# Performance work log

Hardware: AMD Instinct MI355X
Metric: run time of the kernel (lower is better)

Reference implementation:

```python
import jax, jax.numpy as jnp
import numpy as np

GROUPS = 32
EPS = 1e-5


def group_norm(x, scale, bias):
    # x: [B,H,W,C]; stats over (H, W, channels-within-group)
    B, H, W, C = x.shape
    xg = x.reshape(B, H, W, GROUPS, C // GROUPS)
    mean = xg.mean(axis=(1, 2, 4), keepdims=True)
    var = xg.var(axis=(1, 2, 4), keepdims=True)
    xn = ((xg - mean) * jax.lax.rsqrt(var + EPS)).reshape(B, H, W, C)
    return xn * scale + bias


def conv1x1(x, w, b):
    # 1x1 conv == per-pixel matmul; w: [C_in, C_out]
    return jnp.einsum('bhwc,cd->bhwd', x, w) + b


def setup_inputs() -> dict:
    key = jax.random.key(0)
    ks = jax.random.split(key, 10)
    B, H, W, C = 8, 64, 64, 512
    bound = np.sqrt(3.0 / C)  # variance_scaling(1.0, fan_in, uniform)
    x = jax.random.normal(ks[0], (B, H, W, C), dtype=jnp.float32)
    wq = jax.random.uniform(ks[1], (C, C), jnp.float32, -bound, bound)
    wk = jax.random.uniform(ks[2], (C, C), jnp.float32, -bound, bound)
    wv = jax.random.uniform(ks[3], (C, C), jnp.float32, -bound, bound)
    wp = jnp.zeros((C, C), jnp.float32)  # proj_out init scale=0.0
    bq = jnp.zeros((C,), jnp.float32)
    bk = jnp.zeros((C,), jnp.float32)
    bv = jnp.zeros((C,), jnp.float32)
    bp = jnp.zeros((C,), jnp.float32)
    gn_scale = jnp.ones((C,), jnp.float32)
    gn_bias = jnp.zeros((C,), jnp.float32)
    return {"x": x, "wq": wq, "bq": bq, "wk": wk, "bk": bk, "wv": wv,
            "bv": bv, "wp": wp, "bp": bp, "gn_scale": gn_scale, "gn_bias": gn_bias}


def reference(x, wq, bq, wk, bk, wv, bv, wp, bp, gn_scale, gn_bias):
    B, H, W, C = x.shape
    h = group_norm(x, gn_scale, gn_bias)
    q = conv1x1(h, wq, bq).reshape(B, H * W, C)
    k = conv1x1(h, wk, bk).reshape(B, H * W, C)
    v = conv1x1(h, wv, bv).reshape(B, H * W, C)
    # contraction over spatial dim j=H*W -> channel attention [B, C, C]
    attn = jnp.einsum('bji,bjk->bik', q, k)
    attn = jax.nn.softmax(attn, axis=-1)
    h = jnp.einsum('bij,bkj->bik', v, attn)  # [B, HW, C]
    h = h.reshape(B, H, W, C)
    h = conv1x1(h, wp, bp)
    return x + h
```

## Files before the change

### kernel.cpp

```cpp
#include <hip/hip_runtime.h>
#include <hip/hip_bf16.h>


using bf16   = __bf16;
using bf16x8 = __attribute__((ext_vector_type(8))) __bf16;
using bf16x4 = __attribute__((ext_vector_type(4))) __bf16;
using f32x4  = __attribute__((ext_vector_type(4))) float;

#define DI __device__ __forceinline__

DI void gemm128_core(const bf16* __restrict__ A, long lda,
                     const bf16* __restrict__ B, long ldb,
                     int ksteps, bf16* As, bf16* Bs, f32x4 acc[4][4]) {
  const int tid  = threadIdx.x;
  const int lane = tid & 63;
  const int w    = tid >> 6;
  const int lr   = lane & 15;
  const int lk   = (lane >> 4) * 8;
  const int wr   = (w >> 1) * 64;
  const int wc   = (w & 1) * 64;
  const int sw   = (lr & 7) << 3;

  for (int kt = 0; kt < ksteps; ++kt) {
    bf16x8 av[4], bv[4];
#pragma unroll
    for (int c = 0; c < 4; ++c) {
      const int idx = c * 256 + tid;
      const int row = idx >> 3, col = (idx & 7) * 8;
      av[c] = *(const bf16x8*)(A + (long)row * lda + (long)kt * 64 + col);
      bv[c] = *(const bf16x8*)(B + (long)row * ldb + (long)kt * 64 + col);
    }
#pragma unroll
    for (int c = 0; c < 4; ++c) {
      const int idx = c * 256 + tid;
      const int row = idx >> 3;
      const int scol = ((idx & 7) * 8) ^ ((row & 7) << 3);
      *(bf16x8*)(As + row * 64 + scol) = av[c];
      *(bf16x8*)(Bs + row * 64 + scol) = bv[c];
    }
    __syncthreads();
#pragma unroll
    for (int kk = 0; kk < 2; ++kk) {
      bf16x8 af[4], bfr[4];
#pragma unroll
      for (int i = 0; i < 4; ++i)
        af[i] = *(const bf16x8*)(As + (wr + i * 16 + lr) * 64 + ((kk * 32 + lk) ^ sw));
#pragma unroll
      for (int i = 0; i < 4; ++i)
        bfr[i] = *(const bf16x8*)(Bs + (wc + i * 16 + lr) * 64 + ((kk * 32 + lk) ^ sw));
#pragma unroll
      for (int i = 0; i < 4; ++i)
#pragma unroll
        for (int j = 0; j < 4; ++j)
          acc[i][j] = __builtin_amdgcn_mfma_f32_16x16x32_bf16(af[i], bfr[j], acc[i][j], 0, 0, 0);
    }
    __syncthreads();
  }
}

DI void gemm64_core(const bf16* __restrict__ A, long lda,
                    const bf16* __restrict__ B, long ldb,
                    int ksteps, bf16* As, bf16* Bs, f32x4 acc[2][2]) {
  const int tid  = threadIdx.x;
  const int lane = tid & 63;
  const int w    = tid >> 6;
  const int lr   = lane & 15;
  const int lk   = (lane >> 4) * 8;
  const int wr   = (w >> 1) * 32;
  const int wc   = (w & 1) * 32;
  const int sw   = (lr & 7) << 3;

  for (int kt = 0; kt < ksteps; ++kt) {
    bf16x8 av[2], bv[2];
#pragma unroll
    for (int c = 0; c < 2; ++c) {
      const int idx = c * 256 + tid;
      const int row = idx >> 3, col = (idx & 7) * 8;
      av[c] = *(const bf16x8*)(A + (long)row * lda + (long)kt * 64 + col);
      bv[c] = *(const bf16x8*)(B + (long)row * ldb + (long)kt * 64 + col);
    }
#pragma unroll
    for (int c = 0; c < 2; ++c) {
      const int idx = c * 256 + tid;
      const int row = idx >> 3;
      const int scol = ((idx & 7) * 8) ^ ((row & 7) << 3);
      *(bf16x8*)(As + row * 64 + scol) = av[c];
      *(bf16x8*)(Bs + row * 64 + scol) = bv[c];
    }
    __syncthreads();
#pragma unroll
    for (int kk = 0; kk < 2; ++kk) {
      bf16x8 af[2], bfr[2];
#pragma unroll
      for (int i = 0; i < 2; ++i)
        af[i] = *(const bf16x8*)(As + (wr + i * 16 + lr) * 64 + ((kk * 32 + lk) ^ sw));
#pragma unroll
      for (int i = 0; i < 2; ++i)
        bfr[i] = *(const bf16x8*)(Bs + (wc + i * 16 + lr) * 64 + ((kk * 32 + lk) ^ sw));
#pragma unroll
      for (int i = 0; i < 2; ++i)
#pragma unroll
        for (int j = 0; j < 2; ++j)
          acc[i][j] = __builtin_amdgcn_mfma_f32_16x16x32_bf16(af[i], bfr[j], acc[i][j], 0, 0, 0);
    }
    __syncthreads();
  }
}

__global__ __launch_bounds__(256) void k_gnstats(const float* __restrict__ x,
                                                 float2* __restrict__ stats) {
  const int bg = blockIdx.x, b = bg >> 5, g = bg & 31;
  const float* base = x + (size_t)b * 4096 * 512 + g * 16;
  const int tid = threadIdx.x;
  float s = 0.f, ss = 0.f;
  for (int it = 0; it < 64; ++it) {
    const int idx = it * 256 + tid;
    const int p = idx >> 2, c4 = (idx & 3) * 4;
    float4 v = *(const float4*)(base + (size_t)p * 512 + c4);
    s  += v.x + v.y + v.z + v.w;
    ss += v.x * v.x + v.y * v.y + v.z * v.z + v.w * v.w;
  }
  __shared__ float rs[256], rss[256];
  rs[tid] = s; rss[tid] = ss; __syncthreads();
  for (int off = 128; off; off >>= 1) {
    if (tid < off) { rs[tid] += rs[tid + off]; rss[tid] += rss[tid + off]; }
    __syncthreads();
  }
  if (tid == 0) {
    float mean = rs[0] * (1.f / 65536.f);
    float var  = rss[0] * (1.f / 65536.f) - mean * mean;
    stats[bg] = float2{mean, rsqrtf(var + 1e-5f)};
  }
}

__global__ __launch_bounds__(256) void k_gnapply_t(const float* __restrict__ x,
                                                   const float2* __restrict__ stats,
                                                   const float* __restrict__ gns,
                                                   const float* __restrict__ gnb,
                                                   bf16* __restrict__ Hn,
                                                   bf16* __restrict__ HnT,
                                                   float* __restrict__ s) {
  __shared__ bf16 tile[64 * 516];
  __shared__ float cs[512];
  const int tid = threadIdx.x;
  const int blk = blockIdx.x;
  const int b = blk >> 6, p0 = (blk & 63) * 64;
  cs[tid] = 0.f; cs[tid + 256] = 0.f;
  __syncthreads();

  const int c4 = (tid & 127) * 4;
  const int hi = tid >> 7;
  const float2 st = stats[b * 32 + (c4 >> 4)];
  const float4 sc = *(const float4*)(gns + c4);
  const float4 bi = *(const float4*)(gnb + c4);
  float a0 = 0.f, a1 = 0.f, a2 = 0.f, a3 = 0.f;
  for (int i = 0; i < 32; ++i) {
    const int px = i * 2 + hi;
    const float4 xv = *(const float4*)(x + ((size_t)(b * 4096 + p0 + px)) * 512 + c4);
    const float h0 = (xv.x - st.x) * st.y * sc.x + bi.x;
    const float h1 = (xv.y - st.x) * st.y * sc.y + bi.y;
    const float h2 = (xv.z - st.x) * st.y * sc.z + bi.z;
    const float h3 = (xv.w - st.x) * st.y * sc.w + bi.w;
    a0 += h0; a1 += h1; a2 += h2; a3 += h3;
    bf16x4 hv;
    hv[0] = (bf16)h0; hv[1] = (bf16)h1; hv[2] = (bf16)h2; hv[3] = (bf16)h3;
    *(bf16x4*)(Hn + ((size_t)(b * 4096 + p0 + px)) * 512 + c4) = hv;
    *(bf16x4*)(tile + px * 516 + c4) = hv;
  }
  atomicAdd(&cs[c4 + 0], a0); atomicAdd(&cs[c4 + 1], a1);
  atomicAdd(&cs[c4 + 2], a2); atomicAdd(&cs[c4 + 3], a3);
  __syncthreads();
  atomicAdd(s + b * 512 + tid, cs[tid]);
  atomicAdd(s + b * 512 + 256 + tid, cs[tid + 256]);

  for (int cg = 0; cg < 16; ++cg) {
    const int c  = cg * 32 + (tid >> 3);
    const int so = (tid & 7) * 8;
    bf16x8 pk;
#pragma unroll
    for (int k = 0; k < 8; ++k) pk[k] = tile[(so + k) * 516 + c];
    *(bf16x8*)(HnT + ((size_t)(b * 512 + c)) * 4096 + p0 + so) = pk;
  }
}

__global__ void k_wt(const float* __restrict__ wq, const float* __restrict__ wk,
                     const float* __restrict__ wv, const float* __restrict__ wp,
                     bf16* __restrict__ WT, bf16* __restrict__ wvb,
                     float* __restrict__ s) {
  __shared__ float t[32][33];
  const int z = blockIdx.z;
  const float* src = (z == 0) ? wq : (z == 1) ? wk : (z == 2) ? wv : wp;
  const int n0 = blockIdx.x * 32, k0 = blockIdx.y * 32;
  const int tx = threadIdx.x, ty = threadIdx.y;
  if (z == 0 && blockIdx.y == 0) s[blockIdx.x * 256 + ty * 32 + tx] = 0.f;
#pragma unroll
  for (int j = 0; j < 4; ++j) {
    const float v = src[(size_t)(k0 + ty + j * 8) * 512 + n0 + tx];
    t[ty + j * 8][tx] = v;
    if (z == 2) wvb[(size_t)(k0 + ty + j * 8) * 512 + n0 + tx] = (bf16)v;
  }
  __syncthreads();
#pragma unroll
  for (int j = 0; j < 4; ++j)
    WT[(size_t)(z * 512 + n0 + ty + j * 8) * 512 + k0 + tx] = (bf16)t[tx][ty + j * 8];
}

__global__ __launch_bounds__(256) void k_gram(const bf16* __restrict__ HnT,
                                              float* __restrict__ part) {
  __shared__ bf16 As[128 * 64], Bs[128 * 64];
  const int Lb = blockIdx.x;
  const int b  = Lb & 7;
  const int idx = Lb >> 3;
  const int sp = idx & 3;
  const int t  = idx >> 2;
  const int m0 = (int)((0x3221110000ull >> (4 * t)) & 15) * 128;
  const int n0 = (int)((0x3323213210ull >> (4 * t)) & 15) * 128;
  f32x4 acc[4][4];
#pragma unroll
  for (int i = 0; i < 4; ++i)
#pragma unroll
    for (int j = 0; j < 4; ++j) acc[i][j] = (f32x4){0.f, 0.f, 0.f, 0.f};
  const bf16* A = HnT + ((size_t)b * 512 + m0) * 4096 + sp * 1024;
  const bf16* B = HnT + ((size_t)b * 512 + n0) * 4096 + sp * 1024;
  gemm128_core(A, 4096, B, 4096, 16, As, Bs, acc);

  const int lane = threadIdx.x & 63, w = threadIdx.x >> 6;
  const int wr = (w >> 1) * 64, wc = (w & 1) * 64;
  const int rr = (lane >> 4) * 4, cc = lane & 15;
  float* dst = part + (size_t)(sp * 8 + b) * 262144;
#pragma unroll
  for (int i = 0; i < 4; ++i) {
#pragma unroll
    for (int j = 0; j < 4; ++j) {
      const int gm = m0 + wr + i * 16 + rr;
      const int gn = n0 + wc + j * 16 + cc;
      float* p = dst + (size_t)gm * 512 + gn;
      p[0]    = acc[i][j][0];
      p[512]  = acc[i][j][1];
      p[1024] = acc[i][j][2];
      p[1536] = acc[i][j][3];
      if (m0 != n0)
        *(f32x4*)(dst + (size_t)gn * 512 + gm) = acc[i][j];
    }
  }
}

__global__ __launch_bounds__(256) void k_gsum(const float* __restrict__ part,
                                              bf16* __restrict__ G) {
  const size_t S8 = (size_t)8 * 262144;
  const size_t i4 = ((size_t)blockIdx.x * 256 + threadIdx.x) * 4;
  const float4 a = *(const float4*)(part + i4);
  const float4 c = *(const float4*)(part + i4 + S8);
  const float4 d = *(const float4*)(part + i4 + 2 * S8);
  const float4 e = *(const float4*)(part + i4 + 3 * S8);
  bf16x4 o;
  o[0] = (bf16)(a.x + c.x + d.x + e.x); o[1] = (bf16)(a.y + c.y + d.y + e.y);
  o[2] = (bf16)(a.z + c.z + d.z + e.z); o[3] = (bf16)(a.w + c.w + d.w + e.w);
  *(bf16x4*)(G + i4) = o;
}

__global__ __launch_bounds__(512) void k_vecs(const bf16* __restrict__ WT,
                                              const float* __restrict__ s,
                                              const float* __restrict__ bv,
                                              const bf16* __restrict__ T,
                                              float* __restrict__ uq,
                                              float* __restrict__ vkv,
                                              float* __restrict__ dv,
                                              int mode) {
  const int i = threadIdx.x;
  if (mode == 0) {
    const int z = blockIdx.x;
    const int which = z >> 3, b = z & 7;
    const bf16* row = WT + ((size_t)(which * 512 + i)) * 512;
    const float* sv = s + b * 512;
    float acc = 0.f;
    for (int c = 0; c < 512; ++c) acc += (float)row[c] * sv[c];
    (which == 0 ? uq : vkv)[b * 512 + i] = acc;
  } else {
    const int b = blockIdx.x;
    const bf16* row = T + (size_t)b * 262144 + (size_t)i * 512;
    float acc = 0.f;
    for (int c = 0; c < 512; ++c) acc += (float)row[c] * bv[c];
    dv[b * 512 + i] = acc;
  }
}

__global__ __launch_bounds__(256) void k_sg64_bf(const bf16* __restrict__ Ab, long a_bs,
                                                 const bf16* __restrict__ Bb, long b_bs,
                                                 bf16* __restrict__ Cb) {
  __shared__ bf16 As[64 * 64], Bs[64 * 64];
  const int b = blockIdx.z;
  const int m0 = blockIdx.y * 64, n0 = blockIdx.x * 64;
  f32x4 acc[2][2];
#pragma unroll
  for (int i = 0; i < 2; ++i)
#pragma unroll
    for (int j = 0; j < 2; ++j) acc[i][j] = (f32x4){0.f, 0.f, 0.f, 0.f};
  gemm64_core(Ab + (size_t)b * a_bs + (size_t)m0 * 512, 512,
              Bb + (size_t)b * b_bs + (size_t)n0 * 512, 512, 8, As, Bs, acc);

  const int lane = threadIdx.x & 63, w = threadIdx.x >> 6;
  const int wr = (w >> 1) * 32, wc = (w & 1) * 32;
  const int rr = (lane >> 4) * 4, cc = lane & 15;
  bf16* dst = Cb + (size_t)b * 262144;
#pragma unroll
  for (int i = 0; i < 2; ++i) {
#pragma unroll
    for (int j = 0; j < 2; ++j) {
      const int gm = m0 + wr + i * 16 + rr;
      const int gn = n0 + wc + j * 16 + cc;
      bf16* p = dst + (size_t)gm * 512 + gn;
      p[0]    = (bf16)acc[i][j][0];
      p[512]  = (bf16)acc[i][j][1];
      p[1024] = (bf16)acc[i][j][2];
      p[1536] = (bf16)acc[i][j][3];
    }
  }
}

__global__ __launch_bounds__(256) void k_sg64_f32(const bf16* __restrict__ Ab, long a_bs,
                                                  const bf16* __restrict__ Bb, long b_bs,
                                                  float* __restrict__ Cb) {
  __shared__ bf16 As[64 * 64], Bs[64 * 64];
  const int b = blockIdx.z;
  const int m0 = blockIdx.y * 64, n0 = blockIdx.x * 64;
  f32x4 acc[2][2];
#pragma unroll
  for (int i = 0; i < 2; ++i)
#pragma unroll
    for (int j = 0; j < 2; ++j) acc[i][j] = (f32x4){0.f, 0.f, 0.f, 0.f};
  gemm64_core(Ab + (size_t)b * a_bs + (size_t)m0 * 512, 512,
              Bb + (size_t)b * b_bs + (size_t)n0 * 512, 512, 8, As, Bs, acc);

  const int lane = threadIdx.x & 63, w = threadIdx.x >> 6;
  const int wr = (w >> 1) * 32, wc = (w & 1) * 32;
  const int rr = (lane >> 4) * 4, cc = lane & 15;
  float* dst = Cb + (size_t)b * 262144;
#pragma unroll
  for (int i = 0; i < 2; ++i) {
#pragma unroll
    for (int j = 0; j < 2; ++j) {
      const int gm = m0 + wr + i * 16 + rr;
      const int gn = n0 + wc + j * 16 + cc;
      float* p = dst + (size_t)gm * 512 + gn;
      p[0]    = acc[i][j][0];
      p[512]  = acc[i][j][1];
      p[1024] = acc[i][j][2];
      p[1536] = acc[i][j][3];
    }
  }
}

__global__ __launch_bounds__(128) void k_softmax(const float* __restrict__ L,
                                                 const float* __restrict__ uq,
                                                 const float* __restrict__ vkv,
                                                 const float* __restrict__ bq,
                                                 const float* __restrict__ bk,
                                                 bf16* __restrict__ attn) {
  const int row = blockIdx.x, tid = threadIdx.x;
  const int b = row >> 9, i = row & 511;
  const float r  = uq[b * 512 + i];
  const float q0 = bq[i];
  const float4 l  = *(const float4*)(L + (size_t)row * 512 + tid * 4);
  const float4 bk4 = *(const float4*)(bk + tid * 4);
  const float4 vk4 = *(const float4*)(vkv + b * 512 + tid * 4);
  const float v0 = l.x + r * bk4.x + q0 * (vk4.x + 4096.f * bk4.x);
  const float v1 = l.y + r * bk4.y + q0 * (vk4.y + 4096.f * bk4.y);
  const float v2 = l.z + r * bk4.z + q0 * (vk4.z + 4096.f * bk4.z);
  const float v3 = l.w + r * bk4.w + q0 * (vk4.w + 4096.f * bk4.w);
  __shared__ float red[128];
  red[tid] = fmaxf(fmaxf(v0, v1), fmaxf(v2, v3));
  __syncthreads();
  for (int off = 64; off; off >>= 1) {
    if (tid < off) red[tid] = fmaxf(red[tid], red[tid + off]);
    __syncthreads();
  }
  const float M = red[0];
  __syncthreads();
  const float e0 = __expf(v0 - M), e1 = __expf(v1 - M);
  const float e2 = __expf(v2 - M), e3 = __expf(v3 - M);
  red[tid] = e0 + e1 + e2 + e3;
  __syncthreads();
  for (int off = 64; off; off >>= 1) {
    if (tid < off) red[tid] += red[tid + off];
    __syncthreads();
  }
  const float inv = 1.f / red[0];
  bf16x4 o;
  o[0] = (bf16)(e0 * inv); o[1] = (bf16)(e1 * inv);
  o[2] = (bf16)(e2 * inv); o[3] = (bf16)(e3 * inv);
  *(bf16x4*)(attn + (size_t)row * 512 + tid * 4) = o;
}

__global__ void k_att_t(const bf16* __restrict__ attn, bf16* __restrict__ attnT) {
  __shared__ bf16 t[32][33];
  const int b = blockIdx.z;
  const int n0 = blockIdx.x * 32, k0 = blockIdx.y * 32;
  const int tx = threadIdx.x, ty = threadIdx.y;
#pragma unroll
  for (int j = 0; j < 4; ++j)
    t[ty + j * 8][tx] = attn[(size_t)b * 262144 + (size_t)(k0 + ty + j * 8) * 512 + n0 + tx];
  __syncthreads();
#pragma unroll
  for (int j = 0; j < 4; ++j)
    attnT[(size_t)b * 262144 + (size_t)(n0 + ty + j * 8) * 512 + k0 + tx] = t[tx][ty + j * 8];
}

__global__ __launch_bounds__(256) void k_final(const bf16* __restrict__ Hn,
                                               const bf16* __restrict__ CT,
                                               const float* __restrict__ dv,
                                               const float* __restrict__ bp,
                                               const float* __restrict__ x,
                                               float* __restrict__ out) {
  __shared__ bf16 As[128 * 64], Bs[128 * 64];
  const int Lb = blockIdx.x;
  const int b  = Lb & 7;
  const int idx = Lb >> 3;
  const int m0 = (idx >> 2) * 128;
  const int n0 = (idx & 3) * 128;
  f32x4 acc[4][4];
#pragma unroll
  for (int i = 0; i < 4; ++i)
#pragma unroll
    for (int j = 0; j < 4; ++j) acc[i][j] = (f32x4){0.f, 0.f, 0.f, 0.f};
  gemm128_core(Hn + ((size_t)b * 4096 + m0) * 512, 512,
               CT + (size_t)b * 262144 + (size_t)n0 * 512, 512, 8, As, Bs, acc);

  const int lane = threadIdx.x & 63, w = threadIdx.x >> 6;
  const int wr = (w >> 1) * 64, wc = (w & 1) * 64;
  const int rr = (lane >> 4) * 4, cc = lane & 15;
#pragma unroll
  for (int i = 0; i < 4; ++i) {
#pragma unroll
    for (int j = 0; j < 4; ++j) {
      const int gm = m0 + wr + i * 16 + rr;
      const int gn = n0 + wc + j * 16 + cc;
      const float add = dv[b * 512 + gn] + bp[gn];
#pragma unroll
      for (int jj = 0; jj < 4; ++jj) {
        const size_t off = ((size_t)(b * 4096 + gm + jj)) * 512 + gn;
        out[off] = acc[i][j][jj] + add + x[off];
      }
    }
  }
}

extern "C" void kernel_launch(void* const* d_in, const int* in_sizes, int n_in,
                              void* d_out, int out_size, void* d_ws, size_t ws_size,
                              hipStream_t stream) {
  const float* x   = (const float*)d_in[0];
  const float* wq  = (const float*)d_in[1];
  const float* bq  = (const float*)d_in[2];
  const float* wk  = (const float*)d_in[3];
  const float* bk  = (const float*)d_in[4];
  const float* wv  = (const float*)d_in[5];
  const float* bv  = (const float*)d_in[6];
  const float* wp  = (const float*)d_in[7];
  const float* bp  = (const float*)d_in[8];
  const float* gns = (const float*)d_in[9];
  const float* gnb = (const float*)d_in[10];
  float* out = (float*)d_out;

  const size_t MB = 1ull << 20;
  const size_t KB = 1024;
  char* wsb = (char*)d_ws;
  bf16*   WT    = (bf16*)(wsb);
  bf16*   wvb   = (bf16*)(wsb + 2 * MB);
  float2* stats = (float2*)(wsb + 2 * MB + 512 * KB);
  float*  s     = (float*)(wsb + 2 * MB + 576 * KB);
  float*  uq    = (float*)(wsb + 2 * MB + 640 * KB);
  float*  vkv   = (float*)(wsb + 2 * MB + 704 * KB);
  float*  dv    = (float*)(wsb + 2 * MB + 768 * KB);
  bf16*   Hn    = (bf16*)(wsb + 3 * MB);
  bf16*   HnT   = (bf16*)(wsb + 35 * MB);
  float*  part  = (float*)(wsb + 67 * MB);
  bf16*   attn  = (bf16*)(wsb + 67 * MB);
  bf16*   attnT = (bf16*)(wsb + 71 * MB);
  bf16*   T     = (bf16*)(wsb + 75 * MB);
  bf16*   CT    = (bf16*)(wsb + 79 * MB);
  bf16*   G     = (bf16*)(wsb + 99 * MB);
  bf16*   M1    = (bf16*)(wsb + 103 * MB);
  float*  L     = (float*)(wsb + 107 * MB);

  const long S2 = 512 * 512;

  k_wt        <<<dim3(16, 16, 4), dim3(32, 8), 0, stream>>>(wq, wk, wv, wp, WT, wvb, s);
  k_gnstats   <<<dim3(256),       dim3(256),   0, stream>>>(x, stats);
  k_gnapply_t <<<dim3(512),       dim3(256),   0, stream>>>(x, stats, gns, gnb, Hn, HnT, s);
  k_gram      <<<dim3(320),       dim3(256),   0, stream>>>(HnT, part);
  k_gsum      <<<dim3(2048),      dim3(256),   0, stream>>>(part, G);
  k_vecs      <<<dim3(16),        dim3(512),   0, stream>>>(WT, s, bv, T, uq, vkv, dv, 0);
  k_sg64_bf   <<<dim3(8, 8, 8),   dim3(256),   0, stream>>>(WT, 0, G, S2, M1);
  k_sg64_f32  <<<dim3(8, 8, 8),   dim3(256),   0, stream>>>(M1, S2, WT + (size_t)512 * 512, 0, L);
  k_softmax   <<<dim3(4096),      dim3(128),   0, stream>>>(L, uq, vkv, bq, bk, attn);
  k_att_t     <<<dim3(16, 16, 8), dim3(32, 8), 0, stream>>>(attn, attnT);
  k_sg64_bf   <<<dim3(8, 8, 8),   dim3(256),   0, stream>>>(WT + (size_t)3 * 512 * 512, 0, attnT, S2, T);
  k_vecs      <<<dim3(8),         dim3(512),   0, stream>>>(WT, s, bv, T, uq, vkv, dv, 1);
  k_sg64_bf   <<<dim3(8, 8, 8),   dim3(256),   0, stream>>>(T, S2, wvb, 0, CT);
  k_final     <<<dim3(1024),      dim3(256),   0, stream>>>(Hn, CT, dv, bp, x, out);
}
```

Baseline: 195.7 us.

## Fuse prep, gsum/vecs, softmax+transpose; recompute normalized input in final GEMM

Merges the weight transpose and group-norm stats into one launch, folds the row-sum vector products into the G reduction launch, and fuses softmax with the attention transpose while also computing the attn·bv bias term. The final kernel no longer reads a stored bf16 normalized tensor. It recomputes the group-norm from x on the fly and computes the projected bias per block, so the Hn write is dropped. Fewer launches and less global traffic, at the cost of redundant per-block bias dot products and extra fp32 x reads in the final GEMM.

```diff
diff --git a/kernel.cpp b/kernel.cpp
--- a/kernel.cpp
+++ b/kernel.cpp
@@ -107,29 +107,59 @@
   }
 }
 
-__global__ __launch_bounds__(256) void k_gnstats(const float* __restrict__ x,
-                                                 float2* __restrict__ stats) {
-  const int bg = blockIdx.x, b = bg >> 5, g = bg & 31;
-  const float* base = x + (size_t)b * 4096 * 512 + g * 16;
+__global__ __launch_bounds__(256) void k_prep(const float* __restrict__ x,
+                                              const float* __restrict__ wq,
+                                              const float* __restrict__ wk,
+                                              const float* __restrict__ wv,
+                                              const float* __restrict__ wp,
+                                              bf16* __restrict__ WT,
+                                              bf16* __restrict__ wvb,
+                                              float* __restrict__ s,
+                                              float2* __restrict__ stats) {
+  __shared__ float shm[1056];
   const int tid = threadIdx.x;
-  float s = 0.f, ss = 0.f;
-  for (int it = 0; it < 64; ++it) {
-    const int idx = it * 256 + tid;
-    const int p = idx >> 2, c4 = (idx & 3) * 4;
-    float4 v = *(const float4*)(base + (size_t)p * 512 + c4);
-    s  += v.x + v.y + v.z + v.w;
-    ss += v.x * v.x + v.y * v.y + v.z * v.z + v.w * v.w;
-  }
-  __shared__ float rs[256], rss[256];
-  rs[tid] = s; rss[tid] = ss; __syncthreads();
-  for (int off = 128; off; off >>= 1) {
-    if (tid < off) { rs[tid] += rs[tid + off]; rss[tid] += rss[tid + off]; }
-    __syncthreads();
-  }
-  if (tid == 0) {
-    float mean = rs[0] * (1.f / 65536.f);
-    float var  = rss[0] * (1.f / 65536.f) - mean * mean;
-    stats[bg] = float2{mean, rsqrtf(var + 1e-5f)};
+  const int bx = blockIdx.x;
+  if (bx < 256) {
+    const int b = bx >> 5, g = bx & 31;
+    const float* base = x + (size_t)b * 4096 * 512 + g * 16;
+    float sm = 0.f, ss = 0.f;
+    for (int it = 0; it < 64; ++it) {
+      const int idx = it * 256 + tid;
+      const int p = idx >> 2, c4 = (idx & 3) * 4;
+      float4 v = *(const float4*)(base + (size_t)p * 512 + c4);
+      sm += v.x + v.y + v.z + v.w;
+      ss += v.x * v.x + v.y * v.y + v.z * v.z + v.w * v.w;
+    }
+    float* rs = shm; float* rss = shm + 256;
+    rs[tid] = sm; rss[tid] = ss; __syncthreads();
+    for (int off = 128; off; off >>= 1) {
+      if (tid < off) { rs[tid] += rs[tid + off]; rss[tid] += rss[tid + off]; }
+      __syncthreads();
+    }
+    if (tid == 0) {
+      float mean = rs[0] * (1.f / 65536.f);
+      float var  = rss[0] * (1.f / 65536.f) - mean * mean;
+      stats[bx] = float2{mean, rsqrtf(var + 1e-5f)};
+    }
+  } else {
+    const int r = bx - 256;
+    const int z = r >> 8;
+    const int r2 = r & 255;
+    const int bxx = r2 & 15, byy = r2 >> 4;
+    const int tx = tid & 31, ty = tid >> 5;
+    const float* src = (z == 0) ? wq : (z == 1) ? wk : (z == 2) ? wv : wp;
+    const int n0 = bxx * 32, k0 = byy * 32;
+    if (z == 0 && byy == 0) s[bxx * 256 + tid] = 0.f;
+#pragma unroll
+    for (int j = 0; j < 4; ++j) {
+      const float v = src[(size_t)(k0 + ty + j * 8) * 512 + n0 + tx];
+      shm[(ty + j * 8) * 33 + tx] = v;
+      if (z == 2) wvb[(size_t)(k0 + ty + j * 8) * 512 + n0 + tx] = (bf16)v;
+    }
+    __syncthreads();
+#pragma unroll
+    for (int j = 0; j < 4; ++j)
+      WT[(size_t)(z * 512 + n0 + ty + j * 8) * 512 + k0 + tx] = (bf16)shm[tx * 33 + ty + j * 8];
   }
 }
 
@@ -137,7 +167,6 @@
                                                    const float2* __restrict__ stats,
                                                    const float* __restrict__ gns,
                                                    const float* __restrict__ gnb,
-                                                   bf16* __restrict__ Hn,
                                                    bf16* __restrict__ HnT,
                                                    float* __restrict__ s) {
   __shared__ bf16 tile[64 * 516];
@@ -164,7 +193,6 @@
     a0 += h0; a1 += h1; a2 += h2; a3 += h3;
     bf16x4 hv;
     hv[0] = (bf16)h0; hv[1] = (bf16)h1; hv[2] = (bf16)h2; hv[3] = (bf16)h3;
-    *(bf16x4*)(Hn + ((size_t)(b * 4096 + p0 + px)) * 512 + c4) = hv;
     *(bf16x4*)(tile + px * 516 + c4) = hv;
   }
   atomicAdd(&cs[c4 + 0], a0); atomicAdd(&cs[c4 + 1], a1);
@@ -181,28 +209,6 @@
     for (int k = 0; k < 8; ++k) pk[k] = tile[(so + k) * 516 + c];
     *(bf16x8*)(HnT + ((size_t)(b * 512 + c)) * 4096 + p0 + so) = pk;
   }
-}
-
-__global__ void k_wt(const float* __restrict__ wq, const float* __restrict__ wk,
-                     const float* __restrict__ wv, const float* __restrict__ wp,
-                     bf16* __restrict__ WT, bf16* __restrict__ wvb,
-                     float* __restrict__ s) {
-  __shared__ float t[32][33];
-  const int z = blockIdx.z;
-  const float* src = (z == 0) ? wq : (z == 1) ? wk : (z == 2) ? wv : wp;
-  const int n0 = blockIdx.x * 32, k0 = blockIdx.y * 32;
-  const int tx = threadIdx.x, ty = threadIdx.y;
-  if (z == 0 && blockIdx.y == 0) s[blockIdx.x * 256 + ty * 32 + tx] = 0.f;
-#pragma unroll
-  for (int j = 0; j < 4; ++j) {
-    const float v = src[(size_t)(k0 + ty + j * 8) * 512 + n0 + tx];
-    t[ty + j * 8][tx] = v;
-    if (z == 2) wvb[(size_t)(k0 + ty + j * 8) * 512 + n0 + tx] = (bf16)v;
-  }
-  __syncthreads();
-#pragma unroll
-  for (int j = 0; j < 4; ++j)
-    WT[(size_t)(z * 512 + n0 + ty + j * 8) * 512 + k0 + tx] = (bf16)t[tx][ty + j * 8];
 }
 
 __global__ __launch_bounds__(256) void k_gram(const bf16* __restrict__ HnT,
@@ -245,43 +251,41 @@
   }
 }
 
-__global__ __launch_bounds__(256) void k_gsum(const float* __restrict__ part,
-                                              bf16* __restrict__ G) {
-  const size_t S8 = (size_t)8 * 262144;
-  const size_t i4 = ((size_t)blockIdx.x * 256 + threadIdx.x) * 4;
-  const float4 a = *(const float4*)(part + i4);
-  const float4 c = *(const float4*)(part + i4 + S8);
-  const float4 d = *(const float4*)(part + i4 + 2 * S8);
-  const float4 e = *(const float4*)(part + i4 + 3 * S8);
-  bf16x4 o;
-  o[0] = (bf16)(a.x + c.x + d.x + e.x); o[1] = (bf16)(a.y + c.y + d.y + e.y);
-  o[2] = (bf16)(a.z + c.z + d.z + e.z); o[3] = (bf16)(a.w + c.w + d.w + e.w);
-  *(bf16x4*)(G + i4) = o;
-}
-
-__global__ __launch_bounds__(512) void k_vecs(const bf16* __restrict__ WT,
-                                              const float* __restrict__ s,
-                                              const float* __restrict__ bv,
-                                              const bf16* __restrict__ T,
-                                              float* __restrict__ uq,
-                                              float* __restrict__ vkv,
-                                              float* __restrict__ dv,
-                                              int mode) {
-  const int i = threadIdx.x;
-  if (mode == 0) {
-    const int z = blockIdx.x;
+__global__ __launch_bounds__(256) void k_gsumv(const float* __restrict__ part,
+                                               bf16* __restrict__ G,
+                                               const bf16* __restrict__ WT,
+                                               const float* __restrict__ s,
+                                               float* __restrict__ uq,
+                                               float* __restrict__ vkv) {
+  const int bx = blockIdx.x, tid = threadIdx.x;
+  if (bx < 2048) {
+    const size_t S8 = (size_t)8 * 262144;
+    const size_t i4 = ((size_t)bx * 256 + tid) * 4;
+    const float4 a = *(const float4*)(part + i4);
+    const float4 c = *(const float4*)(part + i4 + S8);
+    const float4 d = *(const float4*)(part + i4 + 2 * S8);
+    const float4 e = *(const float4*)(part + i4 + 3 * S8);
+    bf16x4 o;
+    o[0] = (bf16)(a.x + c.x + d.x + e.x); o[1] = (bf16)(a.y + c.y + d.y + e.y);
+    o[2] = (bf16)(a.z + c.z + d.z + e.z); o[3] = (bf16)(a.w + c.w + d.w + e.w);
+    *(bf16x4*)(G + i4) = o;
+  } else {
+    const int z = bx - 2048;
     const int which = z >> 3, b = z & 7;
-    const bf16* row = WT + ((size_t)(which * 512 + i)) * 512;
     const float* sv = s + b * 512;
-    float acc = 0.f;
-    for (int c = 0; c < 512; ++c) acc += (float)row[c] * sv[c];
-    (which == 0 ? uq : vkv)[b * 512 + i] = acc;
-  } else {
-    const int b = blockIdx.x;
-    const bf16* row = T + (size_t)b * 262144 + (size_t)i * 512;
-    float acc = 0.f;
-    for (int c = 0; c < 512; ++c) acc += (float)row[c] * bv[c];
-    dv[b * 512 + i] = acc;
+    for (int o = tid; o < 512; o += 256) {
+      const bf16* row = WT + ((size_t)(which * 512 + o)) * 512;
+      float acc = 0.f;
+      for (int c = 0; c < 512; c += 8) {
+        bf16x8 v = *(const bf16x8*)(row + c);
+        const float4 s0 = *(const float4*)(sv + c);
+        const float4 s1 = *(const float4*)(sv + c + 4);
+        acc += (float)v[0] * s0.x + (float)v[1] * s0.y + (float)v[2] * s0.z +
+               (float)v[3] * s0.w + (float)v[4] * s1.x + (float)v[5] * s1.y +
+               (float)v[6] * s1.z + (float)v[7] * s1.w;
+      }
+      (which == 0 ? uq : vkv)[b * 512 + o] = acc;
+    }
   }
 }
 
@@ -351,91 +355,180 @@
   }
 }
 
-__global__ __launch_bounds__(128) void k_softmax(const float* __restrict__ L,
-                                                 const float* __restrict__ uq,
-                                                 const float* __restrict__ vkv,
-                                                 const float* __restrict__ bq,
-                                                 const float* __restrict__ bk,
-                                                 bf16* __restrict__ attn) {
-  const int row = blockIdx.x, tid = threadIdx.x;
-  const int b = row >> 9, i = row & 511;
+__global__ __launch_bounds__(256) void k_smax(const float* __restrict__ L,
+                                              const float* __restrict__ uq,
+                                              const float* __restrict__ vkv,
+                                              const float* __restrict__ bq,
+                                              const float* __restrict__ bk,
+                                              const float* __restrict__ bv,
+                                              bf16* __restrict__ attnT,
+                                              float* __restrict__ attnbv) {
+  __shared__ bf16 p[4][512];
+  const int tid = threadIdx.x;
+  const int w = tid >> 6, l = tid & 63;
+  const int blk = blockIdx.x;
+  const int gr = blk * 4 + w;
+  const int b = gr >> 9, i = gr & 511;
+  const int c = l * 8;
+
   const float r  = uq[b * 512 + i];
   const float q0 = bq[i];
-  const float4 l  = *(const float4*)(L + (size_t)row * 512 + tid * 4);
-  const float4 bk4 = *(const float4*)(bk + tid * 4);
-  const float4 vk4 = *(const float4*)(vkv + b * 512 + tid * 4);
-  const float v0 = l.x + r * bk4.x + q0 * (vk4.x + 4096.f * bk4.x);
-  const float v1 = l.y + r * bk4.y + q0 * (vk4.y + 4096.f * bk4.y);
-  const float v2 = l.z + r * bk4.z + q0 * (vk4.z + 4096.f * bk4.z);
-  const float v3 = l.w + r * bk4.w + q0 * (vk4.w + 4096.f * bk4.w);
-  __shared__ float red[128];
-  red[tid] = fmaxf(fmaxf(v0, v1), fmaxf(v2, v3));
+  const float* lp = L + (size_t)gr * 512 + c;
+  const float4 l0 = *(const float4*)lp;
+  const float4 l1 = *(const float4*)(lp + 4);
+  const float4 k0 = *(const float4*)(bk + c);
+  const float4 k1 = *(const float4*)(bk + c + 4);
+  const float4 g0 = *(const float4*)(vkv + b * 512 + c);
+  const float4 g1 = *(const float4*)(vkv + b * 512 + c + 4);
+  float v[8];
+  v[0] = l0.x + r * k0.x + q0 * (g0.x + 4096.f * k0.x);
+  v[1] = l0.y + r * k0.y + q0 * (g0.y + 4096.f * k0.y);
+  v[2] = l0.z + r * k0.z + q0 * (g0.z + 4096.f * k0.z);
+  v[3] = l0.w + r * k0.w + q0 * (g0.w + 4096.f * k0.w);
+  v[4] = l1.x + r * k1.x + q0 * (g1.x + 4096.f * k1.x);
+  v[5] = l1.y + r * k1.y + q0 * (g1.y + 4096.f * k1.y);
+  v[6] = l1.z + r * k1.z + q0 * (g1.z + 4096.f * k1.z);
+  v[7] = l1.w + r * k1.w + q0 * (g1.w + 4096.f * k1.w);
+
+  float mx = v[0];
+#pragma unroll
+  for (int j = 1; j < 8; ++j) mx = fmaxf(mx, v[j]);
+  for (int off = 32; off; off >>= 1) mx = fmaxf(mx, __shfl_xor(mx, off));
+  float e[8], sm = 0.f;
+#pragma unroll
+  for (int j = 0; j < 8; ++j) { e[j] = __expf(v[j] - mx); sm += e[j]; }
+  for (int off = 32; off; off >>= 1) sm += __shfl_xor(sm, off);
+  const float inv = 1.f / sm;
+
+  const float4 b0 = *(const float4*)(bv + c);
+  const float4 b1 = *(const float4*)(bv + c + 4);
+  float ab = e[0] * b0.x + e[1] * b0.y + e[2] * b0.z + e[3] * b0.w +
+             e[4] * b1.x + e[5] * b1.y + e[6] * b1.z + e[7] * b1.w;
+  ab *= inv;
+  for (int off = 32; off; off >>= 1) ab += __shfl_xor(ab, off);
+  if (l == 0) attnbv[gr] = ab;
+
+  bf16x8 o;
+#pragma unroll
+  for (int j = 0; j < 8; ++j) o[j] = (bf16)(e[j] * inv);
+  *(bf16x8*)(&p[w][c]) = o;
   __syncthreads();
-  for (int off = 64; off; off >>= 1) {
-    if (tid < off) red[tid] = fmaxf(red[tid], red[tid + off]);
-    __syncthreads();
-  }
-  const float M = red[0];
-  __syncthreads();
-  const float e0 = __expf(v0 - M), e1 = __expf(v1 - M);
-  const float e2 = __expf(v2 - M), e3 = __expf(v3 - M);
-  red[tid] = e0 + e1 + e2 + e3;
-  __syncthreads();
-  for (int off = 64; off; off >>= 1) {
-    if (tid < off) red[tid] += red[tid + off];
-    __syncthreads();
-  }
-  const float inv = 1.f / red[0];
-  bf16x4 o;
-  o[0] = (bf16)(e0 * inv); o[1] = (bf16)(e1 * inv);
-  o[2] = (bf16)(e2 * inv); o[3] = (bf16)(e3 * inv);
-  *(bf16x4*)(attn + (size_t)row * 512 + tid * 4) = o;
-}
-
-__global__ void k_att_t(const bf16* __restrict__ attn, bf16* __restrict__ attnT) {
-  __shared__ bf16 t[32][33];
-  const int b = blockIdx.z;
-  const int n0 = blockIdx.x * 32, k0 = blockIdx.y * 32;
-  const int tx = threadIdx.x, ty = threadIdx.y;
-#pragma unroll
-  for (int j = 0; j < 4; ++j)
-    t[ty + j * 8][tx] = attn[(size_t)b * 262144 + (size_t)(k0 + ty + j * 8) * 512 + n0 + tx];
-  __syncthreads();
-#pragma unroll
-  for (int j = 0; j < 4; ++j)
-    attnT[(size_t)b * 262144 + (size_t)(n0 + ty + j * 8) * 512 + k0 + tx] = t[tx][ty + j * 8];
-}
-
-__global__ __launch_bounds__(256) void k_final(const bf16* __restrict__ Hn,
+
+  const int i0 = (blk * 4) & 511;
+  for (int n = tid; n < 512; n += 256) {
+    bf16x4 t;
+    t[0] = p[0][n]; t[1] = p[1][n]; t[2] = p[2][n]; t[3] = p[3][n];
+    *(bf16x4*)(attnT + (size_t)b * 262144 + (size_t)n * 512 + i0) = t;
+  }
+}
+
+__global__ __launch_bounds__(256) void k_final(const float* __restrict__ x,
                                                const bf16* __restrict__ CT,
-                                               const float* __restrict__ dv,
+                                               const float* __restrict__ attnbv,
+                                               const bf16* __restrict__ WTp,
+                                               const float* __restrict__ gns,
+                                               const float* __restrict__ gnb,
+                                               const float2* __restrict__ stats,
                                                const float* __restrict__ bp,
-                                               const float* __restrict__ x,
                                                float* __restrict__ out) {
   __shared__ bf16 As[128 * 64], Bs[128 * 64];
+  __shared__ float gsc[512], gbs[512], abvs[512], dvs[128];
   const int Lb = blockIdx.x;
   const int b  = Lb & 7;
   const int idx = Lb >> 3;
   const int m0 = (idx >> 2) * 128;
   const int n0 = (idx & 3) * 128;
+  const int tid = threadIdx.x;
+
+  for (int cch = tid; cch < 512; cch += 256) {
+    const float2 st = stats[b * 32 + (cch >> 4)];
+    const float a = st.y * gns[cch];
+    gsc[cch] = a;
+    gbs[cch] = gnb[cch] - st.x * a;
+    abvs[cch] = attnbv[b * 512 + cch];
+  }
+  __syncthreads();
+  if (tid < 128) {
+    const bf16* wrow = WTp + (size_t)(n0 + tid) * 512;
+    float acc = 0.f;
+    for (int k = 0; k < 512; k += 8) {
+      bf16x8 v = *(const bf16x8*)(wrow + k);
+#pragma unroll
+      for (int j = 0; j < 8; ++j) acc += (float)v[j] * abvs[k + j];
+    }
+    dvs[tid] = acc;
+  }
+
+  const int lane = tid & 63, w = tid >> 6;
+  const int lr = lane & 15, lk = (lane >> 4) * 8;
+  const int wr2 = (w >> 1) * 64, wc = (w & 1) * 64;
+  const int sw = (lr & 7) << 3;
   f32x4 acc[4][4];
 #pragma unroll
   for (int i = 0; i < 4; ++i)
 #pragma unroll
     for (int j = 0; j < 4; ++j) acc[i][j] = (f32x4){0.f, 0.f, 0.f, 0.f};
-  gemm128_core(Hn + ((size_t)b * 4096 + m0) * 512, 512,
-               CT + (size_t)b * 262144 + (size_t)n0 * 512, 512, 8, As, Bs, acc);
-
-  const int lane = threadIdx.x & 63, w = threadIdx.x >> 6;
-  const int wr = (w >> 1) * 64, wc = (w & 1) * 64;
+
+  const bf16* Bg = CT + (size_t)b * 262144 + (size_t)n0 * 512;
+  for (int kt = 0; kt < 8; ++kt) {
+    bf16x8 av[4], bv[4];
+#pragma unroll
+    for (int c = 0; c < 4; ++c) {
+      const int idx2 = c * 256 + tid;
+      const int row = idx2 >> 3;
+      const int ch  = kt * 64 + (idx2 & 7) * 8;
+      const float* xp = x + ((size_t)(b * 4096 + m0 + row)) * 512 + ch;
+      const float4 x0 = *(const float4*)xp;
+      const float4 x1 = *(const float4*)(xp + 4);
+      const float4 s0 = *(const float4*)(gsc + ch);
+      const float4 s1 = *(const float4*)(gsc + ch + 4);
+      const float4 c0 = *(const float4*)(gbs + ch);
+      const float4 c1 = *(const float4*)(gbs + ch + 4);
+      av[c][0] = (bf16)(x0.x * s0.x + c0.x);
+      av[c][1] = (bf16)(x0.y * s0.y + c0.y);
+      av[c][2] = (bf16)(x0.z * s0.z + c0.z);
+      av[c][3] = (bf16)(x0.w * s0.w + c0.w);
+      av[c][4] = (bf16)(x1.x * s1.x + c1.x);
+      av[c][5] = (bf16)(x1.y * s1.y + c1.y);
+      av[c][6] = (bf16)(x1.z * s1.z + c1.z);
+      av[c][7] = (bf16)(x1.w * s1.w + c1.w);
+      bv[c] = *(const bf16x8*)(Bg + (size_t)row * 512 + ch);
+    }
+#pragma unroll
+    for (int c = 0; c < 4; ++c) {
+      const int idx2 = c * 256 + tid;
+      const int row = idx2 >> 3;
+      const int scol = ((idx2 & 7) * 8) ^ ((row & 7) << 3);
+      *(bf16x8*)(As + row * 64 + scol) = av[c];
+      *(bf16x8*)(Bs + row * 64 + scol) = bv[c];
+    }
+    __syncthreads();
+#pragma unroll
+    for (int kk = 0; kk < 2; ++kk) {
+      bf16x8 af[4], bfr[4];
+#pragma unroll
+      for (int i = 0; i < 4; ++i)
+        af[i] = *(const bf16x8*)(As + (wr2 + i * 16 + lr) * 64 + ((kk * 32 + lk) ^ sw));
+#pragma unroll
+      for (int i = 0; i < 4; ++i)
+        bfr[i] = *(const bf16x8*)(Bs + (wc + i * 16 + lr) * 64 + ((kk * 32 + lk) ^ sw));
+#pragma unroll
+      for (int i = 0; i < 4; ++i)
+#pragma unroll
+        for (int j = 0; j < 4; ++j)
+          acc[i][j] = __builtin_amdgcn_mfma_f32_16x16x32_bf16(af[i], bfr[j], acc[i][j], 0, 0, 0);
+    }
+    __syncthreads();
+  }
+
   const int rr = (lane >> 4) * 4, cc = lane & 15;
 #pragma unroll
   for (int i = 0; i < 4; ++i) {
 #pragma unroll
     for (int j = 0; j < 4; ++j) {
-      const int gm = m0 + wr + i * 16 + rr;
+      const int gm = m0 + wr2 + i * 16 + rr;
       const int gn = n0 + wc + j * 16 + cc;
-      const float add = dv[b * 512 + gn] + bp[gn];
+      const float add = dvs[gn - n0] + bp[gn];
 #pragma unroll
       for (int jj = 0; jj < 4; ++jj) {
         const size_t off = ((size_t)(b * 4096 + gm + jj)) * 512 + gn;
@@ -464,38 +557,33 @@
   const size_t MB = 1ull << 20;
   const size_t KB = 1024;
   char* wsb = (char*)d_ws;
-  bf16*   WT    = (bf16*)(wsb);
-  bf16*   wvb   = (bf16*)(wsb + 2 * MB);
-  float2* stats = (float2*)(wsb + 2 * MB + 512 * KB);
-  float*  s     = (float*)(wsb + 2 * MB + 576 * KB);
-  float*  uq    = (float*)(wsb + 2 * MB + 640 * KB);
-  float*  vkv   = (float*)(wsb + 2 * MB + 704 * KB);
-  float*  dv    = (float*)(wsb + 2 * MB + 768 * KB);
-  bf16*   Hn    = (bf16*)(wsb + 3 * MB);
-  bf16*   HnT   = (bf16*)(wsb + 35 * MB);
-  float*  part  = (float*)(wsb + 67 * MB);
-  bf16*   attn  = (bf16*)(wsb + 67 * MB);
-  bf16*   attnT = (bf16*)(wsb + 71 * MB);
-  bf16*   T     = (bf16*)(wsb + 75 * MB);
-  bf16*   CT    = (bf16*)(wsb + 79 * MB);
-  bf16*   G     = (bf16*)(wsb + 99 * MB);
-  bf16*   M1    = (bf16*)(wsb + 103 * MB);
-  float*  L     = (float*)(wsb + 107 * MB);
+  bf16*   WT     = (bf16*)(wsb);
+  bf16*   wvb    = (bf16*)(wsb + 2 * MB);
+  float2* stats  = (float2*)(wsb + 2 * MB + 512 * KB);
+  float*  s      = (float*)(wsb + 2 * MB + 576 * KB);
+  float*  uq     = (float*)(wsb + 2 * MB + 640 * KB);
+  float*  vkv    = (float*)(wsb + 2 * MB + 704 * KB);
+  float*  attnbv = (float*)(wsb + 2 * MB + 832 * KB);
+  bf16*   HnT    = (bf16*)(wsb + 35 * MB);
+  float*  part   = (float*)(wsb + 67 * MB);
+  bf16*   attnT  = (bf16*)(wsb + 67 * MB);
+  bf16*   T      = (bf16*)(wsb + 71 * MB);
+  bf16*   CT     = (bf16*)(wsb + 75 * MB);
+  bf16*   G      = (bf16*)(wsb + 99 * MB);
+  bf16*   M1     = (bf16*)(wsb + 103 * MB);
+  float*  L      = (float*)(wsb + 107 * MB);
 
   const long S2 = 512 * 512;
 
-  k_wt        <<<dim3(16, 16, 4), dim3(32, 8), 0, stream>>>(wq, wk, wv, wp, WT, wvb, s);
-  k_gnstats   <<<dim3(256),       dim3(256),   0, stream>>>(x, stats);
-  k_gnapply_t <<<dim3(512),       dim3(256),   0, stream>>>(x, stats, gns, gnb, Hn, HnT, s);
-  k_gram      <<<dim3(320),       dim3(256),   0, stream>>>(HnT, part);
-  k_gsum      <<<dim3(2048),      dim3(256),   0, stream>>>(part, G);
-  k_vecs      <<<dim3(16),        dim3(512),   0, stream>>>(WT, s, bv, T, uq, vkv, dv, 0);
-  k_sg64_bf   <<<dim3(8, 8, 8),   dim3(256),   0, stream>>>(WT, 0, G, S2, M1);
-  k_sg64_f32  <<<dim3(8, 8, 8),   dim3(256),   0, stream>>>(M1, S2, WT + (size_t)512 * 512, 0, L);
-  k_softmax   <<<dim3(4096),      dim3(128),   0, stream>>>(L, uq, vkv, bq, bk, attn);
-  k_att_t     <<<dim3(16, 16, 8), dim3(32, 8), 0, stream>>>(attn, attnT);
-  k_sg64_bf   <<<dim3(8, 8, 8),   dim3(256),   0, stream>>>(WT + (size_t)3 * 512 * 512, 0, attnT, S2, T);
-  k_vecs      <<<dim3(8),         dim3(512),   0, stream>>>(WT, s, bv, T, uq, vkv, dv, 1);
-  k_sg64_bf   <<<dim3(8, 8, 8),   dim3(256),   0, stream>>>(T, S2, wvb, 0, CT);
-  k_final     <<<dim3(1024),      dim3(256),   0, stream>>>(Hn, CT, dv, bp, x, out);
-}
+  k_prep      <<<dim3(1280),    dim3(256), 0, stream>>>(x, wq, wk, wv, wp, WT, wvb, s, stats);
+  k_gnapply_t <<<dim3(512),     dim3(256), 0, stream>>>(x, stats, gns, gnb, HnT, s);
+  k_gram      <<<dim3(320),     dim3(256), 0, stream>>>(HnT, part);
+  k_gsumv     <<<dim3(2064),    dim3(256), 0, stream>>>(part, G, WT, s, uq, vkv);
+  k_sg64_bf   <<<dim3(8, 8, 8), dim3(256), 0, stream>>>(WT, 0, G, S2, M1);
+  k_sg64_f32  <<<dim3(8, 8, 8), dim3(256), 0, stream>>>(M1, S2, WT + (size_t)512 * 512, 0, L);
+  k_smax      <<<dim3(1024),    dim3(256), 0, stream>>>(L, uq, vkv, bq, bk, bv, attnT, attnbv);
+  k_sg64_bf   <<<dim3(8, 8, 8), dim3(256), 0, stream>>>(WT + (size_t)3 * 512 * 512, 0, attnT, S2, T);
+  k_sg64_bf   <<<dim3(8, 8, 8), dim3(256), 0, stream>>>(T, S2, wvb, 0, CT);
+  k_final     <<<dim3(1024),    dim3(256), 0, stream>>>(x, CT, attnbv, WT + (size_t)3 * 512 * 512,
+                                                        gns, gnb, stats, bp, x == nullptr ? nullptr : out);
+}
```

New measurement: 192.2 us. Within noise of the previous version (-1.8%).
